# Optimization experiments

Hardware: AMD Instinct MI355X
Metric: run time of the kernel (lower is better)

## Reference

```python
import jax, jax.numpy as jnp
import numpy as np

SIZE = 20          # nodes per graph instance ('size' expert index)
NUM_CLONE = 2000   # number of cloned graphs in the batch
H = 128            # hidden_dim
L = 3              # num_layers (depth)
N = SIZE * NUM_CLONE
E = NUM_CLONE * SIZE * (SIZE - 1)  # complete digraph per clone
EPS = 1e-5


def _edge_index_np():
    ii, jj = np.meshgrid(np.arange(SIZE), np.arange(SIZE), indexing='ij')
    m = ii != jj
    s, d = ii[m], jj[m]                      # [380] local src/dst
    off = (np.arange(NUM_CLONE) * SIZE)[:, None]
    src = (s[None, :] + off).reshape(-1)
    dst = (d[None, :] + off).reshape(-1)
    return np.stack([src, dst]).astype(np.int32)


def setup_inputs() -> dict:
    key = jax.random.key(0)
    ks = jax.random.split(key, 16)
    s_h = 1.0 / np.sqrt(H)
    s_f = 1.0 / np.sqrt(4 * H)
    inp = {
        'x': jax.random.normal(ks[0], (N, H), jnp.float32),
        'edge_attr': jax.random.normal(ks[1], (E, H), jnp.float32),
        # ResGatedGraphConv params (Linear weights stored as [in, out], bias=False)
        'Wk': jax.random.normal(ks[2], (L, H, H), jnp.float32) * s_h,
        'Wq': jax.random.normal(ks[3], (L, H, H), jnp.float32) * s_h,
        'Wv': jax.random.normal(ks[4], (L, H, H), jnp.float32) * s_h,
        'We': jax.random.normal(ks[5], (L, H, H), jnp.float32) * s_h,
        'Wskip': jax.random.normal(ks[6], (L, H, H), jnp.float32) * s_h,
        # FFN_Expert params (Expert-20), no bias
        'W1': jax.random.normal(ks[7], (L, H, 4 * H), jnp.float32) * s_h,
        'W2': jax.random.normal(ks[8], (L, 4 * H, H), jnp.float32) * s_f,
        # LayerNorm affine params (bias=True)
        'g1': jnp.ones((L, H), jnp.float32),
        'b1': jnp.zeros((L, H), jnp.float32),
        'g2': jnp.ones((L, H), jnp.float32),
        'b2': jnp.zeros((L, H), jnp.float32),
        'edge_index': jnp.asarray(_edge_index_np()),
        'size': SIZE,
    }
    return inp


def _layer_norm(x, g, b):
    mu = jnp.mean(x, axis=-1, keepdims=True)
    var = jnp.mean(jnp.square(x - mu), axis=-1, keepdims=True)
    return (x - mu) * jax.lax.rsqrt(var + EPS) * g + b


def reference(x, edge_attr, Wk, Wq, Wv, We, Wskip, W1, W2, g1, b1, g2, b2, edge_index, size):
    # ConvNetwork: stacked ConvLayer(ResGatedGraph) blocks; dropout=0 (eval)
    src, dst = edge_index[0], edge_index[1]
    n = x.shape[0]
    h = x
    for l in range(L):
        k = h @ Wk[l]                 # [N,H] keys (target role)
        q = h @ Wq[l]                 # [N,H] queries (source role)
        v = h @ Wv[l]                 # [N,H] values (source role)
        e = edge_attr @ We[l]         # [E,H] edge-conditioned term
        gate = jax.nn.sigmoid(k[dst] + q[src] + e)      # [E,H]
        msg = gate * v[src]                              # [E,H]
        agg = jax.ops.segment_sum(msg, dst, num_segments=n)  # scatter-add
        out = agg + h @ Wskip[l]      # skip / root weight
        out = _layer_norm(out, g1[l], b1[l])             # norm1
        # per-size FFN expert (Expert-<size>): Linear->GELU(exact)->Linear
        ffn = jax.nn.gelu(out @ W1[l], approximate=False) @ W2[l]
        h = _layer_norm(out + ffn, g2[l], b2[l])         # norm2
    return h
```

## Files before the change

kernel.cpp:

```cpp
#include <hip/hip_runtime.h>
#include <math.h>

#define NSIZE 20
#define NC 2000
#define H 128
#define NLAYER 3
#define EPB 380
#define NGRP 20

typedef float f32x4 __attribute__((ext_vector_type(4)));
typedef unsigned int u32x4 __attribute__((ext_vector_type(4)));
typedef unsigned short us8 __attribute__((ext_vector_type(8)));
typedef __bf16 bf16x8 __attribute__((ext_vector_type(8)));
typedef unsigned long long u64;

#define OW_E 0
#define OW_K 2048
#define OW_Q 4096
#define OW_V 6144
#define OW_S 8192
#define OW_1 10240
#define OW_2 18432
#define OW_LAYER 26624
#define EA_OFF_B 2097152
#define EA_ELEMS 97280000
#define WS_NEED (EA_OFF_B + (size_t)EA_ELEMS*2)

#define L_HBF   0
#define L_X2    8704
#define L_QARR  8704
#define L_VARR  14304
#define L_BM    25600
#define L_TOT   36160

static __device__ __forceinline__ unsigned short f2bf(float f){
  unsigned u = __float_as_uint(f);
  u += 0x7fffu + ((u >> 16) & 1u);
  return (unsigned short)(u >> 16);
}
static __device__ __forceinline__ float bf2f(unsigned short b){
  return __uint_as_float(((unsigned)b) << 16);
}
static __device__ __forceinline__ unsigned pkbf(float a, float b){
  return (unsigned)f2bf(a) | ((unsigned)f2bf(b) << 16);
}
static __device__ __forceinline__ f32x4 MFMA(u32x4 a, u32x4 b, f32x4 c){
  return __builtin_amdgcn_mfma_f32_16x16x32_bf16(
      __builtin_bit_cast(bf16x8, a), __builtin_bit_cast(bf16x8, b), c, 0, 0, 0);
}
static __device__ __forceinline__ float sigm(float x){
  return __builtin_amdgcn_rcpf(1.f + __expf(-x));
}

__global__ __launch_bounds__(256) void pack_weights(
    const float* __restrict__ Wk, const float* __restrict__ Wq,
    const float* __restrict__ Wv, const float* __restrict__ We,
    const float* __restrict__ Ws, const float* __restrict__ W1,
    const float* __restrict__ W2, u32x4* __restrict__ outp)
{
  int l = blockIdx.x / 7, m = blockIdx.x % 7;
  const float* src; int K, N; long base;
  switch(m){
    case 0: src = We + (long)l*H*H;   K=H;   N=H;   base=OW_E; break;
    case 1: src = Wk + (long)l*H*H;   K=H;   N=H;   base=OW_K; break;
    case 2: src = Wq + (long)l*H*H;   K=H;   N=H;   base=OW_Q; break;
    case 3: src = Wv + (long)l*H*H;   K=H;   N=H;   base=OW_V; break;
    case 4: src = Ws + (long)l*H*H;   K=H;   N=H;   base=OW_S; break;
    case 5: src = W1 + (long)l*H*4*H; K=H;   N=4*H; base=OW_1; break;
    default: src = W2 + (long)l*4*H*H; K=4*H; N=H;  base=OW_2; break;
  }
  base += (long)l * OW_LAYER;
  int KT = K/32, NT = N/16;
  int total = KT*NT*64;
  for(int i = threadIdx.x; i < total; i += 256){
    int lane = i & 63, f = i >> 6;
    int kt = f % KT, nt = f / KT;
    int col = nt*16 + (lane & 15);
    int k0 = kt*32 + (lane >> 4)*8;
    us8 v;
    #pragma unroll
    for(int j=0;j<8;++j) v[j] = f2bf(src[(long)(k0+j)*N + col]);
    outp[base + (long)f*64 + lane] = __builtin_bit_cast(u32x4, v);
  }
}

template<bool EAB>
__global__ __launch_bounds__(256, 4) void moe_gnn(
    const float* __restrict__ x, const float* __restrict__ ea,
    unsigned short* __restrict__ eab,
    const float* __restrict__ g1, const float* __restrict__ b1,
    const float* __restrict__ g2, const float* __restrict__ b2,
    const u32x4* __restrict__ wp, float* __restrict__ out)
{
  __shared__ __align__(16) unsigned char smem[L_TOT];
  unsigned short* hbf  = (unsigned short*)(smem + L_HBF);
  unsigned short* x2   = (unsigned short*)(smem + L_X2);
  unsigned short* qarr = (unsigned short*)(smem + L_QARR);
  unsigned short* varr = (unsigned short*)(smem + L_VARR);
  float*          Bm   = (float*)(smem + L_BM);

  const int c   = blockIdx.x;
  const int tid = threadIdx.x;
  const int w   = tid >> 6;
  const int l   = tid & 63;
  const int lg  = l >> 4;
  const int l15 = l & 15;
  const long cEPB = (long)c * EPB;

  if(EAB){
    const f32x4* src = (const f32x4*)(ea + cEPB*H);
    u32x4* dst = (u32x4*)(eab + cEPB*H);
    for(int i = tid; i < EPB*H/8; i += 256){
      f32x4 a = __builtin_nontemporal_load(&src[2*i]);
      f32x4 b = __builtin_nontemporal_load(&src[2*i+1]);
      dst[i] = (u32x4){ pkbf(a[0],a[1]), pkbf(a[2],a[3]),
                        pkbf(b[0],b[1]), pkbf(b[2],b[3]) };
    }
  }
  for(int i = tid; i < 32*H; i += 256){
    int r = i >> 7, cc = i & 127;
    float v = (r < NSIZE) ? x[((long)c*NSIZE + r)*H + cc] : 0.f;
    hbf[r*136 + cc] = f2bf(v);
  }
  __syncthreads();

  #pragma unroll 1
  for(int layer = 0; layer < NLAYER; ++layer){
    const u32x4* wl = wp + (long)layer*OW_LAYER;
    f32x4 kreg[2][2];
    f32x4 agg[2][2];

    {
      u32x4 hb[2][4];
      #pragma unroll
      for(int nt=0; nt<2; ++nt)
        #pragma unroll
        for(int kt=0; kt<4; ++kt)
          hb[nt][kt] = *(const u32x4*)&hbf[(nt*16+l15)*136 + kt*32 + lg*8];

      #pragma unroll
      for(int m=0; m<4; ++m){
        const long ow = (m==0?OW_K: m==1?OW_Q: m==2?OW_V: OW_S);
        #pragma unroll
        for(int mt=0; mt<2; ++mt)
          #pragma unroll
          for(int nt=0; nt<2; ++nt){
            f32x4 acc = {0.f,0.f,0.f,0.f};
            #pragma unroll
            for(int kt=0; kt<4; ++kt)
              acc = MFMA(wl[ow + (((2*w+mt)*4)+kt)*64 + l], hb[nt][kt], acc);
            if(m==0) kreg[mt][nt] = acc;
            else if(m==3) agg[mt][nt] = acc;
            else {
              unsigned short* dst = (m==1) ? qarr : varr;
              if(nt==0 || l15 < 4){
                u64 pk = (u64)pkbf(acc[0],acc[1]) | ((u64)pkbf(acc[2],acc[3]) << 32);
                *(u64*)&dst[(nt*16+l15)*140 + (2*w+mt)*16 + lg*4] = pk;
              }
            }
          }
      }
    }

    {
      u32x4 eB[2][4];
      #pragma unroll
      for(int mt=0;mt<2;++mt)
        #pragma unroll
        for(int kt=0;kt<4;++kt)
          eB[mt][kt] = wl[OW_E + ((2*w+mt)*4+kt)*64 + l];

      #pragma unroll 2
      for(int g=0; g<NGRP; ++g){
        bool va = (l15 != g);
        int s = l15 - ((l15 > g) ? 1 : 0);
        long row = cEPB + (long)g*19 + (va ? s : 0);
        u32x4 ef[4];
        if(EAB){
          const unsigned short* ep = eab + row*H + lg*8;
          #pragma unroll
          for(int kt=0;kt<4;++kt) ef[kt] = *(const u32x4*)(ep + kt*32);
        } else {
          const float* ap = ea + row*H + lg*8;
          #pragma unroll
          for(int kt=0;kt<4;++kt){
            f32x4 lo = *(const f32x4*)(ap + kt*32);
            f32x4 hi = *(const f32x4*)(ap + kt*32 + 4);
            ef[kt] = (u32x4){ pkbf(lo[0],lo[1]), pkbf(lo[2],lo[3]),
                              pkbf(hi[0],hi[1]), pkbf(hi[2],hi[3]) };
          }
        }
        #pragma unroll
        for(int mt=0; mt<2; ++mt){
          u64 q8 = *(const u64*)&qarr[g*140 + (2*w+mt)*16 + lg*4];
          u64 v8 = *(const u64*)&varr[g*140 + (2*w+mt)*16 + lg*4];
          f32x4 acc = {0.f,0.f,0.f,0.f};
          #pragma unroll
          for(int kt=0;kt<4;++kt)
            acc = MFMA(eB[mt][kt], ef[kt], acc);
          #pragma unroll
          for(int j=0;j<4;++j){
            float q_ = bf2f((unsigned short)(q8 >> (16*j)));
            float v_ = bf2f((unsigned short)(v8 >> (16*j)));
            float xg = acc[j] + kreg[mt][0][j] + q_;
            float m_ = sigm(xg) * v_;
            agg[mt][0][j] += va ? m_ : 0.f;
          }
        }
      }

      {
        const int qi = l15 >> 2, di = l15 & 3;
        f32x4 aggR[2];
        aggR[0] = (f32x4){0.f,0.f,0.f,0.f};
        aggR[1] = (f32x4){0.f,0.f,0.f,0.f};
        #pragma unroll 1
        for(int qb=0; qb<NGRP; qb+=4){
          int g = qb + qi;
          int d = 16 + di;
          bool va = (d != g);
          int s = d - ((d > g) ? 1 : 0);
          long row = cEPB + (long)g*19 + (va ? s : 0);
          u32x4 ef[4];
          if(EAB){
            const unsigned short* ep = eab + row*H + lg*8;
            #pragma unroll
            for(int kt=0;kt<4;++kt) ef[kt] = *(const u32x4*)(ep + kt*32);
          } else {
            const float* ap = ea + row*H + lg*8;
            #pragma unroll
            for(int kt=0;kt<4;++kt){
              f32x4 lo = *(const f32x4*)(ap + kt*32);
              f32x4 hi = *(const f32x4*)(ap + kt*32 + 4);
              ef[kt] = (u32x4){ pkbf(lo[0],lo[1]), pkbf(lo[2],lo[3]),
                                pkbf(hi[0],hi[1]), pkbf(hi[2],hi[3]) };
            }
          }
          #pragma unroll
          for(int mt=0; mt<2; ++mt){
            u64 q8 = *(const u64*)&qarr[g*140 + (2*w+mt)*16 + lg*4];
            u64 v8 = *(const u64*)&varr[g*140 + (2*w+mt)*16 + lg*4];
            f32x4 acc = {0.f,0.f,0.f,0.f};
            #pragma unroll
            for(int kt=0;kt<4;++kt)
              acc = MFMA(eB[mt][kt], ef[kt], acc);
            #pragma unroll
            for(int j=0;j<4;++j){
              float kk = __shfl(kreg[mt][1][j], (lg<<4) | di, 64);
              float q_ = bf2f((unsigned short)(q8 >> (16*j)));
              float v_ = bf2f((unsigned short)(v8 >> (16*j)));
              float xg = acc[j] + kk + q_;
              float m_ = sigm(xg) * v_;
              aggR[mt][j] += va ? m_ : 0.f;
            }
          }
        }
        #pragma unroll
        for(int mt=0; mt<2; ++mt)
          #pragma unroll
          for(int j=0;j<4;++j){
            float t = aggR[mt][j];
            t += __shfl_xor(t, 4, 64);
            t += __shfl_xor(t, 8, 64);
            agg[mt][1][j] += t;
          }
      }

      #pragma unroll
      for(int nt=0; nt<2; ++nt)
        if(nt==0 || l15 < 4)
          #pragma unroll
          for(int mt=0; mt<2; ++mt)
            *(f32x4*)&Bm[(nt*16+l15)*132 + (2*w+mt)*16 + lg*4] = agg[mt][nt];
    }
    __syncthreads();

    {
      const float* gp = g1 + layer*H; const float* bp = b1 + layer*H;
      float gv0 = gp[l], gv1 = gp[64+l], bv0 = bp[l], bv1 = bp[64+l];
      for(int i=0;i<5;++i){
        int r = w + 4*i;
        float v0 = Bm[r*132 + l], v1 = Bm[r*132 + 64 + l];
        float s = v0+v1;
        #pragma unroll
        for(int m=1;m<64;m<<=1) s += __shfl_xor(s, m, 64);
        float mu = s*(1.f/128.f);
        float d0=v0-mu, d1=v1-mu;
        float qv = d0*d0 + d1*d1;
        #pragma unroll
        for(int m=1;m<64;m<<=1) qv += __shfl_xor(qv, m, 64);
        float rs = rsqrtf(qv*(1.f/128.f) + 1e-5f);
        float y0 = d0*rs*gv0 + bv0;
        float y1 = d1*rs*gv1 + bv1;
        Bm[r*132 + l] = y0; Bm[r*132 + 64 + l] = y1;
        hbf[r*136 + l] = f2bf(y0); hbf[r*136 + 64 + l] = f2bf(y1);
      }
    }
    __syncthreads();

    {
      u32x4 hb2[2][4];
      #pragma unroll
      for(int nt=0;nt<2;++nt)
        #pragma unroll
        for(int kt=0;kt<4;++kt)
          hb2[nt][kt] = *(const u32x4*)&hbf[(nt*16+l15)*136 + kt*32 + lg*8];
      f32x4 c2[2][2];
      #pragma unroll
      for(int mt=0;mt<2;++mt)
        #pragma unroll
        for(int nt=0;nt<2;++nt)
          c2[mt][nt] = (f32x4){0.f,0.f,0.f,0.f};
      #pragma unroll 1
      for(int hh=0; hh<2; ++hh){
        for(int i2=0;i2<4;++i2){
          int mtg = hh*16 + w*4 + i2;
          #pragma unroll
          for(int nt=0;nt<2;++nt){
            f32x4 acc = {0.f,0.f,0.f,0.f};
            #pragma unroll
            for(int kt=0;kt<4;++kt)
              acc = MFMA(wl[OW_1 + (mtg*4+kt)*64 + l], hb2[nt][kt], acc);
            float ge[4];
            #pragma unroll
            for(int j=0;j<4;++j){
              float v = acc[j];
              float u = v*(0.7978845608f + 0.0356774081f*v*v);
              ge[j] = v * sigm(2.f*u);
            }
            u64 pk = (u64)pkbf(ge[0],ge[1]) | ((u64)pkbf(ge[2],ge[3]) << 32);
            *(u64*)&x2[(nt*16+l15)*264 + (w*4+i2)*16 + lg*4] = pk;
          }
        }
        __syncthreads();
        #pragma unroll
        for(int nt=0;nt<2;++nt){
          #pragma unroll
          for(int kt=0;kt<8;++kt){
            u32x4 xb = *(const u32x4*)&x2[(nt*16+l15)*264 + kt*32 + lg*8];
            #pragma unroll
            for(int mt=0;mt<2;++mt)
              c2[mt][nt] = MFMA(wl[OW_2 + ((2*w+mt)*16 + hh*8 + kt)*64 + l],
                                xb, c2[mt][nt]);
          }
        }
        __syncthreads();
      }
      #pragma unroll
      for(int nt=0;nt<2;++nt)
        if(nt==0 || l15 < 4)
          #pragma unroll
          for(int mt=0;mt<2;++mt){
            float* p = &Bm[(nt*16+l15)*132 + (2*w+mt)*16 + lg*4];
            *(f32x4*)p = *(f32x4*)p + c2[mt][nt];
          }
    }
    __syncthreads();

    {
      const float* gp = g2 + layer*H; const float* bp = b2 + layer*H;
      float gv0 = gp[l], gv1 = gp[64+l], bv0 = bp[l], bv1 = bp[64+l];
      for(int i=0;i<5;++i){
        int r = w + 4*i;
        float v0 = Bm[r*132 + l], v1 = Bm[r*132 + 64 + l];
        float s = v0+v1;
        #pragma unroll
        for(int m=1;m<64;m<<=1) s += __shfl_xor(s, m, 64);
        float mu = s*(1.f/128.f);
        float d0=v0-mu, d1=v1-mu;
        float qv = d0*d0 + d1*d1;
        #pragma unroll
        for(int m=1;m<64;m<<=1) qv += __shfl_xor(qv, m, 64);
        float rs = rsqrtf(qv*(1.f/128.f) + 1e-5f);
        float y0 = d0*rs*gv0 + bv0;
        float y1 = d1*rs*gv1 + bv1;
        hbf[r*136 + l] = f2bf(y0); hbf[r*136 + 64 + l] = f2bf(y1);
        if(layer == NLAYER-1){
          __builtin_nontemporal_store(y0, &out[((long)c*NSIZE + r)*H + l]);
          __builtin_nontemporal_store(y1, &out[((long)c*NSIZE + r)*H + 64 + l]);
        }
      }
    }
    __syncthreads();
  }
}

extern "C" void kernel_launch(void* const* d_in, const int* in_sizes, int n_in,
                              void* d_out, int out_size, void* d_ws, size_t ws_size,
                              hipStream_t stream) {
  const float* x  = (const float*)d_in[0];
  const float* ea = (const float*)d_in[1];
  const float* Wk = (const float*)d_in[2];
  const float* Wq = (const float*)d_in[3];
  const float* Wv = (const float*)d_in[4];
  const float* We = (const float*)d_in[5];
  const float* Ws = (const float*)d_in[6];
  const float* W1 = (const float*)d_in[7];
  const float* W2 = (const float*)d_in[8];
  const float* g1 = (const float*)d_in[9];
  const float* b1 = (const float*)d_in[10];
  const float* g2 = (const float*)d_in[11];
  const float* b2 = (const float*)d_in[12];
  u32x4* wp = (u32x4*)d_ws;

  hipLaunchKernelGGL(pack_weights, dim3(21), dim3(256), 0, stream,
                     Wk, Wq, Wv, We, Ws, W1, W2, wp);
  if(ws_size >= WS_NEED){
    unsigned short* eab = (unsigned short*)((char*)d_ws + EA_OFF_B);
    hipLaunchKernelGGL(moe_gnn<true>, dim3(NC), dim3(256), 0, stream,
                       x, ea, eab, g1, b1, g2, b2, wp, (float*)d_out);
  } else {
    hipLaunchKernelGGL(moe_gnn<false>, dim3(NC), dim3(256), 0, stream,
                       x, ea, (unsigned short*)nullptr,
                       g1, b1, g2, b2, wp, (float*)d_out);
  }
}
```

Measured before the change: 582.7 us.

## Pre-permute bf16 edge fragments and stream via async global-to-LDS double buffer

The bf16 edge-attribute cache is now written in MFMA fragment order per clone, including the duplicate diagonal rows needed by the gather pattern, instead of plain row-major. In later layers the main edge loop streams these fragments with global_load_lds into a double-buffered LDS staging area, with one block barrier per group, and the remainder loop reads contiguous fragments. The aim is coalesced 16-byte loads and overlap of global fetch with MFMA and sigmoid work. In exchange it adds 20 block barriers per layer, writes slightly more workspace, and does gather address arithmetic during the first pass.

```diff
diff --git a/kernel.cpp b/kernel.cpp
--- a/kernel.cpp
+++ b/kernel.cpp
@@ -23,8 +23,9 @@
 #define OW_2 18432
 #define OW_LAYER 26624
 #define EA_OFF_B 2097152
-#define EA_ELEMS 97280000
-#define WS_NEED (EA_OFF_B + (size_t)EA_ELEMS*2)
+#define FM_MAIN_B 81920
+#define FM_CLONE_B 102400
+#define WS_NEED (EA_OFF_B + (size_t)NC*FM_CLONE_B)
 
 #define L_HBF   0
 #define L_X2    8704
@@ -50,6 +51,11 @@
 }
 static __device__ __forceinline__ float sigm(float x){
   return __builtin_amdgcn_rcpf(1.f + __expf(-x));
+}
+static __device__ __forceinline__ void gload_lds16(const void* g, void* l){
+  __builtin_amdgcn_global_load_lds(
+      (const __attribute__((address_space(1))) unsigned int*)g,
+      (__attribute__((address_space(3))) unsigned int*)l, 16, 0, 0);
 }
 
 __global__ __launch_bounds__(256) void pack_weights(
@@ -98,6 +104,7 @@
   unsigned short* qarr = (unsigned short*)(smem + L_QARR);
   unsigned short* varr = (unsigned short*)(smem + L_VARR);
   float*          Bm   = (float*)(smem + L_BM);
+  unsigned char*  stb  = (unsigned char*)(smem + L_BM);
 
   const int c   = blockIdx.x;
   const int tid = threadIdx.x;
@@ -106,15 +113,31 @@
   const int lg  = l >> 4;
   const int l15 = l & 15;
   const long cEPB = (long)c * EPB;
+  const char* gsrc = (const char*)eab + (long)c*FM_CLONE_B;
 
   if(EAB){
-    const f32x4* src = (const f32x4*)(ea + cEPB*H);
-    u32x4* dst = (u32x4*)(eab + cEPB*H);
-    for(int i = tid; i < EPB*H/8; i += 256){
-      f32x4 a = __builtin_nontemporal_load(&src[2*i]);
-      f32x4 b = __builtin_nontemporal_load(&src[2*i+1]);
-      dst[i] = (u32x4){ pkbf(a[0],a[1]), pkbf(a[2],a[3]),
-                        pkbf(b[0],b[1]), pkbf(b[2],b[3]) };
+    u32x4* fm = (u32x4*)gsrc;
+    const int WMAIN = NGRP*4*64;
+    const int WTOT  = WMAIN + 5*4*64;
+    for(int widx = tid; widx < WTOT; widx += 256){
+      int g, s, kt, lidx;
+      if(widx < WMAIN){
+        g = widx >> 8; kt = (widx >> 6) & 3; lidx = widx & 63;
+        int d = lidx & 15;
+        s = (d == g) ? 0 : (d - (d > g ? 1 : 0));
+      } else {
+        int wr = widx - WMAIN;
+        int b4 = wr >> 8; kt = (wr >> 6) & 3; lidx = wr & 63;
+        int qi = (lidx & 15) >> 2, di = lidx & 3;
+        g = b4*4 + qi; int d = 16 + di;
+        s = (d == g) ? 0 : (d - (d > g ? 1 : 0));
+      }
+      int lgx = lidx >> 4;
+      const float* sp = ea + (cEPB + (long)g*19 + s)*H + kt*32 + lgx*8;
+      f32x4 a = *(const f32x4*)sp;
+      f32x4 b = *(const f32x4*)(sp + 4);
+      fm[widx] = (u32x4){ pkbf(a[0],a[1]), pkbf(a[2],a[3]),
+                          pkbf(b[0],b[1]), pkbf(b[2],b[3]) };
     }
   }
   for(int i = tid; i < 32*H; i += 256){
@@ -170,18 +193,47 @@
         for(int kt=0;kt<4;++kt)
           eB[mt][kt] = wl[OW_E + ((2*w+mt)*4+kt)*64 + l];
 
-      #pragma unroll 2
-      for(int g=0; g<NGRP; ++g){
-        bool va = (l15 != g);
-        int s = l15 - ((l15 > g) ? 1 : 0);
-        long row = cEPB + (long)g*19 + (va ? s : 0);
-        u32x4 ef[4];
-        if(EAB){
-          const unsigned short* ep = eab + row*H + lg*8;
-          #pragma unroll
-          for(int kt=0;kt<4;++kt) ef[kt] = *(const u32x4*)(ep + kt*32);
-        } else {
+      if(EAB){
+        gload_lds16(gsrc + (long)w*1024 + (long)l*16, stb + w*1024);
+        __syncthreads();
+        #pragma unroll 1
+        for(int g=0; g<NGRP; ++g){
+          if(g+1 < NGRP)
+            gload_lds16(gsrc + (long)(g+1)*4096 + w*1024 + (long)l*16,
+                        stb + ((g+1)&1)*4096 + w*1024);
+          const unsigned char* sb = stb + (g&1)*4096;
+          u32x4 ef[4];
+          #pragma unroll
+          for(int kt=0;kt<4;++kt)
+            ef[kt] = *(const u32x4*)(sb + kt*1024 + l*16);
+          bool va = (l15 != g);
+          #pragma unroll
+          for(int mt=0; mt<2; ++mt){
+            u64 q8 = *(const u64*)&qarr[g*140 + (2*w+mt)*16 + lg*4];
+            u64 v8 = *(const u64*)&varr[g*140 + (2*w+mt)*16 + lg*4];
+            f32x4 acc = {0.f,0.f,0.f,0.f};
+            #pragma unroll
+            for(int kt=0;kt<4;++kt)
+              acc = MFMA(eB[mt][kt], ef[kt], acc);
+            #pragma unroll
+            for(int j=0;j<4;++j){
+              float q_ = bf2f((unsigned short)(q8 >> (16*j)));
+              float v_ = bf2f((unsigned short)(v8 >> (16*j)));
+              float xg = acc[j] + kreg[mt][0][j] + q_;
+              float m_ = sigm(xg) * v_;
+              agg[mt][0][j] += va ? m_ : 0.f;
+            }
+          }
+          __syncthreads();
+        }
+      } else {
+        #pragma unroll 2
+        for(int g=0; g<NGRP; ++g){
+          bool va = (l15 != g);
+          int s = l15 - ((l15 > g) ? 1 : 0);
+          long row = cEPB + (long)g*19 + (va ? s : 0);
           const float* ap = ea + row*H + lg*8;
+          u32x4 ef[4];
           #pragma unroll
           for(int kt=0;kt<4;++kt){
             f32x4 lo = *(const f32x4*)(ap + kt*32);
@@ -189,22 +241,22 @@
             ef[kt] = (u32x4){ pkbf(lo[0],lo[1]), pkbf(lo[2],lo[3]),
                               pkbf(hi[0],hi[1]), pkbf(hi[2],hi[3]) };
           }
-        }
-        #pragma unroll
-        for(int mt=0; mt<2; ++mt){
-          u64 q8 = *(const u64*)&qarr[g*140 + (2*w+mt)*16 + lg*4];
-          u64 v8 = *(const u64*)&varr[g*140 + (2*w+mt)*16 + lg*4];
-          f32x4 acc = {0.f,0.f,0.f,0.f};
-          #pragma unroll
-          for(int kt=0;kt<4;++kt)
-            acc = MFMA(eB[mt][kt], ef[kt], acc);
-          #pragma unroll
-          for(int j=0;j<4;++j){
-            float q_ = bf2f((unsigned short)(q8 >> (16*j)));
-            float v_ = bf2f((unsigned short)(v8 >> (16*j)));
-            float xg = acc[j] + kreg[mt][0][j] + q_;
-            float m_ = sigm(xg) * v_;
-            agg[mt][0][j] += va ? m_ : 0.f;
+          #pragma unroll
+          for(int mt=0; mt<2; ++mt){
+            u64 q8 = *(const u64*)&qarr[g*140 + (2*w+mt)*16 + lg*4];
+            u64 v8 = *(const u64*)&varr[g*140 + (2*w+mt)*16 + lg*4];
+            f32x4 acc = {0.f,0.f,0.f,0.f};
+            #pragma unroll
+            for(int kt=0;kt<4;++kt)
+              acc = MFMA(eB[mt][kt], ef[kt], acc);
+            #pragma unroll
+            for(int j=0;j<4;++j){
+              float q_ = bf2f((unsigned short)(q8 >> (16*j)));
+              float v_ = bf2f((unsigned short)(v8 >> (16*j)));
+              float xg = acc[j] + kreg[mt][0][j] + q_;
+              float m_ = sigm(xg) * v_;
+              agg[mt][0][j] += va ? m_ : 0.f;
+            }
           }
         }
       }
@@ -214,19 +266,20 @@
         f32x4 aggR[2];
         aggR[0] = (f32x4){0.f,0.f,0.f,0.f};
         aggR[1] = (f32x4){0.f,0.f,0.f,0.f};
+        const u32x4* rfm = (const u32x4*)(gsrc + FM_MAIN_B);
         #pragma unroll 1
-        for(int qb=0; qb<NGRP; qb+=4){
-          int g = qb + qi;
+        for(int b4=0; b4<5; ++b4){
+          int g = b4*4 + qi;
           int d = 16 + di;
           bool va = (d != g);
-          int s = d - ((d > g) ? 1 : 0);
-          long row = cEPB + (long)g*19 + (va ? s : 0);
           u32x4 ef[4];
           if(EAB){
-            const unsigned short* ep = eab + row*H + lg*8;
-            #pragma unroll
-            for(int kt=0;kt<4;++kt) ef[kt] = *(const u32x4*)(ep + kt*32);
+            #pragma unroll
+            for(int kt=0;kt<4;++kt)
+              ef[kt] = rfm[b4*256 + kt*64 + l];
           } else {
+            int s = d - ((d > g) ? 1 : 0);
+            long row = cEPB + (long)g*19 + (va ? s : 0);
             const float* ap = ea + row*H + lg*8;
             #pragma unroll
             for(int kt=0;kt<4;++kt){
```

Result: no change. 592.9 us (+1.8%).
